# Kernel tuning notes

Hardware: AMD Instinct MI355X
Metric: run time of the kernel (lower is better)

## Reference

```python
import jax, jax.numpy as jnp
import numpy as np

N_NODES = 100000
N_EDGES = 600000
DIM = 128
NUM_CLASSES = 10
NUM_GRAPHS = 512
NUM_LAYERS = 4
BN_EPS = 1e-5


def _bn(h, g, b):
    # BatchNorm1d, training-mode statistics (biased variance), affine
    m = h.mean(axis=0)
    v = jnp.var(h, axis=0)
    return (h - m) * jax.lax.rsqrt(v + BN_EPS) * g + b


def setup_inputs() -> dict:
    key = jax.random.key(0)
    ks = jax.random.split(key, 8)
    s_in = 1.0 / np.sqrt(DIM)
    x = jax.random.normal(ks[0], (N_NODES, DIM), dtype=jnp.float32)
    edge_index = jax.random.randint(ks[1], (2, N_EDGES), 0, N_NODES, dtype=jnp.int32)
    batch = jnp.sort(jax.random.randint(ks[2], (N_NODES,), 0, NUM_GRAPHS, dtype=jnp.int32))
    return {
        "x": x,
        "edge_index": edge_index,
        "batch": batch,
        "mlp_w1": jax.random.normal(ks[3], (NUM_LAYERS, DIM, DIM), dtype=jnp.float32) * s_in,
        "mlp_b1": jnp.zeros((NUM_LAYERS, DIM), dtype=jnp.float32),
        "mlp_bn_g": jnp.ones((NUM_LAYERS, DIM), dtype=jnp.float32),
        "mlp_bn_b": jnp.zeros((NUM_LAYERS, DIM), dtype=jnp.float32),
        "mlp_w2": jax.random.normal(ks[4], (NUM_LAYERS, DIM, DIM), dtype=jnp.float32) * s_in,
        "mlp_b2": jnp.zeros((NUM_LAYERS, DIM), dtype=jnp.float32),
        "bn_g": jnp.ones((NUM_LAYERS, DIM), dtype=jnp.float32),
        "bn_b": jnp.zeros((NUM_LAYERS, DIM), dtype=jnp.float32),
        "fc_w": jax.random.normal(ks[5], (NUM_LAYERS + 1, DIM, NUM_CLASSES), dtype=jnp.float32) * s_in,
        "fc_b": jnp.zeros((NUM_LAYERS + 1, NUM_CLASSES), dtype=jnp.float32),
    }


def reference(x, edge_index, batch, mlp_w1, mlp_b1, mlp_bn_g, mlp_bn_b,
              mlp_w2, mlp_b2, bn_g, bn_b, fc_w, fc_b):
    src, dst = edge_index[0], edge_index[1]
    outs = [x]
    h = x
    for i in range(NUM_LAYERS):
        # GINConv: (1+eps)*x + sum_{j in N(i)} x_j  with eps=0 (default)
        agg = jax.ops.segment_sum(h[src], dst, num_segments=N_NODES)
        z = h + agg
        # nn.Sequential(Linear, BatchNorm1d, ReLU, Linear)
        z = jax.nn.relu(_bn(z @ mlp_w1[i] + mlp_b1[i], mlp_bn_g[i], mlp_bn_b[i]))
        z = z @ mlp_w2[i] + mlp_b2[i]
        # outer BN + ReLU
        h = jax.nn.relu(_bn(z, bn_g[i], bn_b[i]))
        outs.append(h)
    out = None
    for i, o in enumerate(outs):
        pooled = jax.ops.segment_sum(o, batch, num_segments=NUM_GRAPHS)
        y = pooled @ fc_w[i] + fc_b[i]  # dropout is identity in eval mode
        out = y if out is None else out + y
    return jax.nn.log_softmax(out, axis=-1)
```

## Files before the change

kernel.cpp:

```cpp
#include <hip/hip_runtime.h>

#define NN 100000
#define NE 600000
#define DD 128
#define NG 512
#define NC 10
#define NL 4

typedef __attribute__((ext_vector_type(8))) short short8;
typedef __attribute__((ext_vector_type(4))) float f32x4;
typedef __attribute__((ext_vector_type(4))) unsigned int u32x4;

__device__ __forceinline__ float b2f(unsigned int u) { return __uint_as_float(u << 16); }
__device__ __forceinline__ unsigned int f2b(float f) {
    unsigned int u = __float_as_uint(f);
    return (u + 0x7fffu + ((u >> 16) & 1u)) >> 16;
}
__device__ __forceinline__ void unpack8(uint4 v, float* f) {
    f[0] = b2f(v.x & 0xffffu); f[1] = b2f(v.x >> 16);
    f[2] = b2f(v.y & 0xffffu); f[3] = b2f(v.y >> 16);
    f[4] = b2f(v.z & 0xffffu); f[5] = b2f(v.z >> 16);
    f[6] = b2f(v.w & 0xffffu); f[7] = b2f(v.w >> 16);
}
__device__ __forceinline__ uint4 pack8(const float* f) {
    uint4 v;
    v.x = f2b(f[0]) | (f2b(f[1]) << 16);
    v.y = f2b(f[2]) | (f2b(f[3]) << 16);
    v.z = f2b(f[4]) | (f2b(f[5]) << 16);
    v.w = f2b(f[6]) | (f2b(f[7]) << 16);
    return v;
}
__device__ __forceinline__ void nt_store16(uint4 v, ushort* p) {
    u32x4 w = {v.x, v.y, v.z, v.w};
    __builtin_nontemporal_store(w, (u32x4*)p);
}

__device__ __forceinline__ void gload_lds16(const void* g, void* l) {
    __builtin_amdgcn_global_load_lds((__attribute__((address_space(1))) void*)g,
                                     (__attribute__((address_space(3))) void*)l, 16, 0, 0);
}

__device__ __forceinline__ void build_bnp(const float* __restrict__ st, const float* __restrict__ gma,
                                          const float* __restrict__ bta, float (*bnp)[DD], int t) {
    if (t < DD) {
        float s = 0.f, q = 0.f;
        #pragma unroll
        for (int r = 0; r < 8; ++r) { s += st[r * DD + t]; q += st[8 * DD + r * DD + t]; }
        const float invn = 1.0f / NN;
        float m = s * invn;
        float var = q * invn - m * m;
        float sc = gma[t] * rsqrtf(var + 1e-5f);
        bnp[0][t] = sc;
        bnp[1][t] = bta[t] - m * sc;
    }
}

__global__ __launch_bounds__(256) void k_init(const float* __restrict__ x, ushort* __restrict__ h,
                                              float* __restrict__ pz, int nz, int* __restrict__ deg,
                                              const float* __restrict__ w1, const float* __restrict__ w2,
                                              ushort* __restrict__ wp) {
    const int T = gridDim.x * 256;
    const int tid = blockIdx.x * 256 + threadIdx.x;
    for (int i = tid; i < NN * DD / 8; i += T) {
        float4 a = ((const float4*)x)[2 * i], b = ((const float4*)x)[2 * i + 1];
        float f[8] = {a.x, a.y, a.z, a.w, b.x, b.y, b.z, b.w};
        ((uint4*)h)[i] = pack8(f);
    }
    for (int i = tid; i < nz; i += T) pz[i] = 0.f;
    for (int i = tid; i < NN; i += T) deg[i] = 0;
    for (int id = tid; id < 16384; id += T) {
        int v = id & 63;
        int kc = (id >> 6) & 3;
        int ct = (id >> 8) & 7;
        int m = id >> 11;
        const float* W = (m < 4) ? (w1 + (size_t)m * DD * DD) : (w2 + (size_t)(m - 4) * DD * DD);
        int c = ct * 16 + (v & 15);
        int kbase = kc * 32 + ((v >> 4) << 3);
        ushort* dst = wp + ((size_t)id << 3);
        #pragma unroll
        for (int j = 0; j < 8; ++j) dst[j] = (ushort)f2b(W[(size_t)(kbase + j) * DD + c]);
    }
}


__global__ __launch_bounds__(256) void k_hist(const int* __restrict__ dst, int* __restrict__ deg) {
    int e = blockIdx.x * 256 + threadIdx.x;
    if (e < NE) atomicAdd(&deg[dst[e]], 1);
}
__global__ __launch_bounds__(256) void k_partial(const int* __restrict__ deg, int* __restrict__ part) {
    __shared__ int s[256];
    int t = threadIdx.x;
    int i = blockIdx.x * 256 + t;
    s[t] = (i < NN) ? deg[i] : 0;
    __syncthreads();
    #pragma unroll
    for (int off = 128; off >= 1; off >>= 1) {
        if (t < off) s[t] += s[t + off];
        __syncthreads();
    }
    if (t == 0) part[blockIdx.x] = s[0];
}
__global__ __launch_bounds__(512) void k_scanpart(int* __restrict__ part, int nb) {
    __shared__ int s[512];
    int t = threadIdx.x;
    int v = (t < nb) ? part[t] : 0;
    s[t] = v;
    __syncthreads();
    #pragma unroll
    for (int off = 1; off < 512; off <<= 1) {
        int add = (t >= off) ? s[t - off] : 0;
        __syncthreads();
        s[t] += add;
        __syncthreads();
    }
    if (t < nb) part[t] = s[t] - v;
}
__global__ __launch_bounds__(256) void k_exscan(const int* __restrict__ deg, const int* __restrict__ part,
                                                int* __restrict__ rowofs, int* __restrict__ cursor) {
    __shared__ int s[256];
    int b = blockIdx.x, t = threadIdx.x;
    int i = b * 256 + t;
    int v = (i < NN) ? deg[i] : 0;
    s[t] = v;
    __syncthreads();
    #pragma unroll
    for (int off = 1; off < 256; off <<= 1) {
        int add = (t >= off) ? s[t - off] : 0;
        __syncthreads();
        s[t] += add;
        __syncthreads();
    }
    if (i < NN) {
        int r = part[b] + s[t] - v;
        rowofs[i] = r;
        cursor[i] = r;
    }
    if (i == NN - 1) rowofs[NN] = part[b] + s[t];
}
__global__ __launch_bounds__(256) void k_fill(const int* __restrict__ src, const int* __restrict__ dst,
                                              int* __restrict__ cursor, int* __restrict__ csr) {
    int e = blockIdx.x * 256 + threadIdx.x;
    if (e >= NE) return;
    int d = dst[e];
    int pos = atomicAdd(&cursor[d], 1);
    csr[pos] = src[e];
}

template<bool BN>
__global__ __launch_bounds__(256) void k_gather(const int* __restrict__ rowofs, const int* __restrict__ csr,
                                                const int* __restrict__ batch,
                                                const ushort* __restrict__ h, ushort* __restrict__ z,
                                                const float* __restrict__ st, const float* __restrict__ gma,
                                                const float* __restrict__ bta,
                                                float* __restrict__ poolslot) {
    __shared__ float bnp[2][DD];
    __shared__ float sfl[16][DD];
    __shared__ int gids[16];
    int t = threadIdx.x;
    if (BN) build_bnp(st, gma, bta, bnp, t);
    int rs = t >> 4;
    int n = blockIdx.x * 16 + rs;
    int cl = t & 15;
    int cb = cl * 8;
    if (cl == 0) gids[rs] = batch[n];
    uint4 v = ((const uint4*)h)[(size_t)n * 16 + cl];
    if (BN) __syncthreads();
    float sc[8], sh[8];
    if (BN) {
        #pragma unroll
        for (int j = 0; j < 8; ++j) { sc[j] = bnp[0][cb + j]; sh[j] = bnp[1][cb + j]; }
    }
    float acc[8], f[8];
    unpack8(v, f);
    #pragma unroll
    for (int j = 0; j < 8; ++j)
        acc[j] = BN ? fmaxf(fmaf(f[j], sc[j], sh[j]), 0.f) : f[j];
    #pragma unroll
    for (int j = 0; j < 8; j += 4)
        *(float4*)(&sfl[rs][cb + j]) = make_float4(acc[j], acc[j + 1], acc[j + 2], acc[j + 3]);
    __syncthreads();
    if (t < DD) {
        float run = sfl[0][t];
        int gprev = gids[0];
        #pragma unroll
        for (int s = 1; s < 16; ++s) {
            int gg = gids[s];
            float vv = sfl[s][t];
            if (gg != gprev) {
                atomicAdd(poolslot + (size_t)gprev * DD + t, run);
                run = 0.f;
                gprev = gg;
            }
            run += vv;
        }
        atomicAdd(poolslot + (size_t)gprev * DD + t, run);
    }
    int e = rowofs[n], end = rowofs[n + 1];
    int i0 = 0, i1 = 0, i2 = 0, i3 = 0;
    if (e + 3 < end) { i0 = csr[e]; i1 = csr[e + 1]; i2 = csr[e + 2]; i3 = csr[e + 3]; }
    while (e + 3 < end) {
        uint4 v0 = ((const uint4*)h)[(size_t)i0 * 16 + cl];
        uint4 v1 = ((const uint4*)h)[(size_t)i1 * 16 + cl];
        uint4 v2 = ((const uint4*)h)[(size_t)i2 * 16 + cl];
        uint4 v3 = ((const uint4*)h)[(size_t)i3 * 16 + cl];
        int en = e + 4;
        if (en + 3 < end) {
            i0 = csr[en]; i1 = csr[en + 1]; i2 = csr[en + 2]; i3 = csr[en + 3];
        }
        float f0[8], f1[8], f2[8], f3[8];
        unpack8(v0, f0); unpack8(v1, f1); unpack8(v2, f2); unpack8(v3, f3);
        #pragma unroll
        for (int j = 0; j < 8; ++j) {
            float a0 = BN ? fmaxf(fmaf(f0[j], sc[j], sh[j]), 0.f) : f0[j];
            float a1 = BN ? fmaxf(fmaf(f1[j], sc[j], sh[j]), 0.f) : f1[j];
            float a2 = BN ? fmaxf(fmaf(f2[j], sc[j], sh[j]), 0.f) : f2[j];
            float a3 = BN ? fmaxf(fmaf(f3[j], sc[j], sh[j]), 0.f) : f3[j];
            acc[j] += (a0 + a1) + (a2 + a3);
        }
        e = en;
    }
    for (; e < end; ++e) {
        uint4 v0 = ((const uint4*)h)[(size_t)csr[e] * 16 + cl];
        float f0[8];
        unpack8(v0, f0);
        #pragma unroll
        for (int j = 0; j < 8; ++j)
            acc[j] += BN ? fmaxf(fmaf(f0[j], sc[j], sh[j]), 0.f) : f0[j];
    }
    nt_store16(pack8(acc), z + ((size_t)n * 16 + cl) * 8);
}

template<bool TRANS>
__global__ __launch_bounds__(256, 4) void k_mm(const ushort* __restrict__ in, const ushort* __restrict__ wp,
                                               const float* __restrict__ bias,
                                               const float* __restrict__ stin, const float* __restrict__ gma,
                                               const float* __restrict__ bta,
                                               ushort* __restrict__ outp, float* __restrict__ stout) {
    __shared__ __align__(16) char lds[16384];
    __shared__ float bnp[2][DD];
    const int t = threadIdx.x;
    const int lane = t & 63;
    const int wid = t >> 6;
    const int wr = wid >> 1, wc = wid & 1;
    const int rb = blockIdx.x * 64;
    const int rep = blockIdx.x & 7;

    if (TRANS) {
        build_bnp(stin, gma, bta, bnp, t);
        __syncthreads();
    }
    if (!TRANS && rb + 64 <= NN) {
        #pragma unroll
        for (int i = 0; i < 4; ++i) {
            int p = i * 256 + t;
            int row = p >> 4;
            int oc = (p & 15) ^ (row & 7);
            gload_lds16((const uint4*)in + (size_t)(rb + row) * 16 + oc, lds + p * 16);
        }
    } else {
        float scv[8], shv[8];
        if (TRANS) {
            int cb = (t & 15) * 8;
            #pragma unroll
            for (int j = 0; j < 8; ++j) { scv[j] = bnp[0][cb + j]; shv[j] = bnp[1][cb + j]; }
        }
        #pragma unroll
        for (int i = 0; i < 4; ++i) {
            int c = i * 256 + t;
            int row = c >> 4;
            int g = rb + row;
            uint4 v = make_uint4(0, 0, 0, 0);
            if (g < NN) {
                v = *((const uint4*)in + (size_t)g * 16 + (c & 15));
                if (TRANS) {
                    float f[8];
                    unpack8(v, f);
                    #pragma unroll
                    for (int j = 0; j < 8; ++j) f[j] = fmaxf(fmaf(f[j], scv[j], shv[j]), 0.f);
                    v = pack8(f);
                }
            }
            *(uint4*)(lds + ((c * 16) ^ ((row & 7) << 4))) = v;
        }
    }
    __syncthreads();

    f32x4 acc[2][4];
    #pragma unroll
    for (int rt = 0; rt < 2; ++rt)
        #pragma unroll
        for (int ct = 0; ct < 4; ++ct) acc[rt][ct] = (f32x4){0.f, 0.f, 0.f, 0.f};

    #pragma unroll
    for (int kc = 0; kc < 4; ++kc) {
        short8 wf[4];
        #pragma unroll
        for (int ct = 0; ct < 4; ++ct)
            wf[ct] = *(const short8*)(wp + (size_t)((((wc * 4 + ct) * 4 + kc) * 64 + lane) << 3));
        #pragma unroll
        for (int rt = 0; rt < 2; ++rt) {
            int row = wr * 32 + rt * 16 + (lane & 15);
            int off = (row * 256 + ((kc * 32 + ((lane >> 4) << 3)) << 1)) ^ ((row & 7) << 4);
            short8 zf = *(const short8*)(lds + off);
            #pragma unroll
            for (int ct = 0; ct < 4; ++ct)
                acc[rt][ct] = __builtin_amdgcn_mfma_f32_16x16x32_bf16(wf[ct], zf, acc[rt][ct], 0, 0, 0);
        }
    }
    __syncthreads();

    const int zr = lane & 15, cq = lane >> 4;
    #pragma unroll
    for (int rt = 0; rt < 2; ++rt) {
        int row = wr * 32 + rt * 16 + zr;
        #pragma unroll
        for (int ct = 0; ct < 4; ++ct) {
            int c0 = wc * 64 + ct * 16 + cq * 4;
            float4 bi = *(const float4*)(bias + c0);
            f32x4 a = acc[rt][ct];
            uint2 pk;
            pk.x = f2b(a[0] + bi.x) | (f2b(a[1] + bi.y) << 16);
            pk.y = f2b(a[2] + bi.z) | (f2b(a[3] + bi.w) << 16);
            *(uint2*)(lds + ((row * 256 + c0 * 2) ^ ((row & 7) << 4))) = pk;
        }
    }
    __syncthreads();

    float s8[8], q8[8];
    #pragma unroll
    for (int j = 0; j < 8; ++j) { s8[j] = 0.f; q8[j] = 0.f; }
    #pragma unroll
    for (int i = 0; i < 4; ++i) {
        int c = i * 256 + t;
        int row = c >> 4;
        int g = rb + row;
        if (g < NN) {
            uint4 v = *(const uint4*)(lds + ((c * 16) ^ ((row & 7) << 4)));
            ((uint4*)outp)[(size_t)g * 16 + (c & 15)] = v;
            float f[8];
            unpack8(v, f);
            #pragma unroll
            for (int j = 0; j < 8; ++j) { s8[j] += f[j]; q8[j] += f[j] * f[j]; }
        }
    }
    #pragma unroll
    for (int j = 0; j < 8; ++j) {
        s8[j] += __shfl_xor(s8[j], 16); s8[j] += __shfl_xor(s8[j], 32);
        q8[j] += __shfl_xor(q8[j], 16); q8[j] += __shfl_xor(q8[j], 32);
    }
    __syncthreads();
    float* rs2 = (float*)lds;
    if (lane < 16) {
        #pragma unroll
        for (int j = 0; j < 8; j += 4) {
            *(float4*)(rs2 + wid * DD + lane * 8 + j) = make_float4(s8[j], s8[j+1], s8[j+2], s8[j+3]);
            *(float4*)(rs2 + 4 * DD + wid * DD + lane * 8 + j) = make_float4(q8[j], q8[j+1], q8[j+2], q8[j+3]);
        }
    }
    __syncthreads();
    if (t < DD) {
        float s = rs2[t] + rs2[DD + t] + rs2[2 * DD + t] + rs2[3 * DD + t];
        float q = rs2[4 * DD + t] + rs2[5 * DD + t] + rs2[6 * DD + t] + rs2[7 * DD + t];
        atomicAdd(stout + rep * DD + t, s);
        atomicAdd(stout + 8 * DD + rep * DD + t, q);
    }
}

__device__ __forceinline__ int lowerb(const int* __restrict__ a, int n, int key) {
    int lo = 0, hi = n;
    while (lo < hi) {
        int mid = (lo + hi) >> 1;
        if (a[mid] < key) lo = mid + 1; else hi = mid;
    }
    return lo;
}

__global__ __launch_bounds__(256) void k_poolread(const int* __restrict__ batch, const ushort* __restrict__ h,
                                                  const float* __restrict__ pooled,
                                                  const float* __restrict__ st, const float* __restrict__ gma,
                                                  const float* __restrict__ bta,
                                                  const float* __restrict__ fcw, const float* __restrict__ fcb,
                                                  float* __restrict__ out) {
    __shared__ float bnp[2][DD];
    __shared__ float red[16 * DD];
    __shared__ float ps[2][NC];
    int t = threadIdx.x;
    build_bnp(st, gma, bta, bnp, t);
    __syncthreads();
    int g = blockIdx.x;
    int cl = t & 15;
    int rs = t >> 4;
    int cb = cl * 8;
    float sc[8], sh[8];
    #pragma unroll
    for (int j = 0; j < 8; ++j) { sc[j] = bnp[0][cb + j]; sh[j] = bnp[1][cb + j]; }
    int start = lowerb(batch, NN, g);
    int end = lowerb(batch, NN, g + 1);
    float acc[8];
    #pragma unroll
    for (int j = 0; j < 8; ++j) acc[j] = 0.f;
    for (int n = start + rs; n < end; n += 16) {
        uint4 v = ((const uint4*)h)[(size_t)n * 16 + cl];
        float f[8];
        unpack8(v, f);
        #pragma unroll
        for (int j = 0; j < 8; ++j)
            acc[j] += fmaxf(fmaf(f[j], sc[j], sh[j]), 0.f);
    }
    #pragma unroll
    for (int j = 0; j < 8; j += 4)
        *(float4*)(red + rs * DD + cb + j) = make_float4(acc[j], acc[j + 1], acc[j + 2], acc[j + 3]);
    __syncthreads();
    #pragma unroll
    for (int off = 8; off >= 1; off >>= 1) {
        if (rs < off) {
            #pragma unroll
            for (int j = 0; j < 8; j += 4) {
                float4 a = *(float4*)(red + rs * DD + cb + j);
                float4 b = *(float4*)(red + (rs + off) * DD + cb + j);
                a.x += b.x; a.y += b.y; a.z += b.z; a.w += b.w;
                *(float4*)(red + rs * DD + cb + j) = a;
            }
        }
        __syncthreads();
    }
    if (t < DD) {
        int d = t;
        float part[NC];
        #pragma unroll
        for (int c = 0; c < NC; ++c) part[c] = 0.f;
        #pragma unroll
        for (int i = 0; i < NL; ++i) {
            float v = pooled[((size_t)i * NG + g) * DD + d];
            const float* wr = fcw + ((size_t)i * DD + d) * NC;
            #pragma unroll
            for (int c = 0; c < NC; ++c) part[c] = fmaf(v, wr[c], part[c]);
        }
        {
            float v = red[d];
            const float* wr = fcw + ((size_t)NL * DD + d) * NC;
            #pragma unroll
            for (int c = 0; c < NC; ++c) part[c] = fmaf(v, wr[c], part[c]);
        }
        #pragma unroll
        for (int off = 32; off >= 1; off >>= 1) {
            #pragma unroll
            for (int c = 0; c < NC; ++c) part[c] += __shfl_down(part[c], off);
        }
        if ((t & 63) == 0) {
            #pragma unroll
            for (int c = 0; c < NC; ++c) ps[t >> 6][c] = part[c];
        }
    }
    __syncthreads();
    if (t == 0) {
        float y[NC];
        #pragma unroll
        for (int c = 0; c < NC; ++c) {
            float bs = 0.f;
            for (int i = 0; i < NL + 1; ++i) bs += fcb[i * NC + c];
            y[c] = ps[0][c] + ps[1][c] + bs;
        }
        float m = y[0];
        #pragma unroll
        for (int c = 1; c < NC; ++c) m = fmaxf(m, y[c]);
        float sum = 0.f;
        #pragma unroll
        for (int c = 0; c < NC; ++c) sum += expf(y[c] - m);
        float ls = logf(sum);
        #pragma unroll
        for (int c = 0; c < NC; ++c) out[(size_t)g * NC + c] = y[c] - m - ls;
    }
}


extern "C" void kernel_launch(void* const* d_in, const int* in_sizes, int n_in,
                              void* d_out, int out_size, void* d_ws, size_t ws_size,
                              hipStream_t stream) {
    const float* x   = (const float*)d_in[0];
    const int*   ei  = (const int*)d_in[1];
    const int*   bat = (const int*)d_in[2];
    const float* w1  = (const float*)d_in[3];
    const float* b1  = (const float*)d_in[4];
    const float* mbg = (const float*)d_in[5];
    const float* mbb = (const float*)d_in[6];
    const float* w2  = (const float*)d_in[7];
    const float* b2  = (const float*)d_in[8];
    const float* bng = (const float*)d_in[9];
    const float* bnb = (const float*)d_in[10];
    const float* fcw = (const float*)d_in[11];
    const float* fcb = (const float*)d_in[12];
    float* out = (float*)d_out;

    ushort* H  = (ushort*)d_ws;
    ushort* Z  = H + (size_t)NN * DD;
    ushort* Y1 = Z + (size_t)NN * DD;
    ushort* WP = Y1 + (size_t)NN * DD;
    float* pooled = (float*)(WP + 8 * 16384);
    float* stats  = pooled + (size_t)NL * NG * DD;
    int* deg    = (int*)(stats + 8 * 16 * DD);
    int* rowofs = deg + NN;
    int* part   = rowofs + NN + 1;
    int* cursor = part + 512;
    int* csr    = cursor + NN;

    const int* src = ei;
    const int* dst = ei + NE;
    const int nbN = (NN + 255) / 256;
    const int nbE = (NE + 255) / 256;
    const int nzero = NL * NG * DD + 8 * 16 * DD;

    hipLaunchKernelGGL(k_init, dim3(NN * DD / 8 / 256 + 1), dim3(256), 0, stream,
                       x, H, pooled, nzero, deg, w1, w2, WP);
    hipLaunchKernelGGL(k_hist, dim3(nbE), dim3(256), 0, stream, dst, deg);
    hipLaunchKernelGGL(k_partial, dim3(nbN), dim3(256), 0, stream, deg, part);
    hipLaunchKernelGGL(k_scanpart, dim3(1), dim3(512), 0, stream, part, nbN);
    hipLaunchKernelGGL(k_exscan, dim3(nbN), dim3(256), 0, stream, deg, part, rowofs, cursor);
    hipLaunchKernelGGL(k_fill, dim3(nbE), dim3(256), 0, stream, src, dst, cursor, csr);

    const int gmm = (NN + 63) / 64;
    const int ggt = NN / 16;
    const int SLOT = 16 * DD;
    for (int i = 0; i < NL; ++i) {
        float* st_mlp = stats + (size_t)(2 * i + 0) * SLOT;
        float* st_out = stats + (size_t)(2 * i + 1) * SLOT;
        const float* st_prev = stats + (size_t)(2 * i - 1) * SLOT;
        float* poolslot = pooled + (size_t)i * NG * DD;
        if (i == 0) {
            hipLaunchKernelGGL((k_gather<false>), dim3(ggt), dim3(256), 0, stream, rowofs, csr, bat, H, Z,
                               (const float*)nullptr, (const float*)nullptr, (const float*)nullptr, poolslot);
        } else {
            hipLaunchKernelGGL((k_gather<true>), dim3(ggt), dim3(256), 0, stream, rowofs, csr, bat, H, Z,
                               st_prev, bng + (size_t)(i - 1) * DD, bnb + (size_t)(i - 1) * DD, poolslot);
        }
        hipLaunchKernelGGL((k_mm<false>), dim3(gmm), dim3(256), 0, stream,
                           Z, WP + (size_t)i * 16384, b1 + (size_t)i * DD,
                           (const float*)nullptr, (const float*)nullptr, (const float*)nullptr,
                           Y1, st_mlp);
        hipLaunchKernelGGL((k_mm<true>), dim3(gmm), dim3(256), 0, stream,
                           Y1, WP + (size_t)(4 + i) * 16384, b2 + (size_t)i * DD,
                           st_mlp, mbg + (size_t)i * DD, mbb + (size_t)i * DD,
                           H, st_out);
    }
    hipLaunchKernelGGL(k_poolread, dim3(NG), dim3(256), 0, stream, bat, H, pooled,
                       stats + (size_t)7 * SLOT, bng + (size_t)3 * DD, bnb + (size_t)3 * DD,
                       fcw, fcb, out);
}
```

Baseline: 369.3 us.

## Fuse both MLP matmuls into one cooperative kernel with grid-wide BN sync

Each of the two per-layer MLP matmuls becomes one cooperative kernel. A block computes the first linear layer for 128 rows and keeps the bf16 result in LDS. A grid sync then waits for the global BatchNorm statistics, and the block applies BN plus ReLU in LDS before the second matmul. This removes the global write and re-read of the intermediate activation and one launch per layer. In exchange it needs every block resident at once, pays for a grid-wide barrier, and falls back to the two-kernel path if the cooperative launch fails.

```diff
diff --git a/kernel.cpp b/kernel.cpp
--- a/kernel.cpp
+++ b/kernel.cpp
@@ -1,4 +1,5 @@
 #include <hip/hip_runtime.h>
+#include <hip/hip_cooperative_groups.h>
 
 #define NN 100000
 #define NE 600000
@@ -6,6 +7,8 @@
 #define NG 512
 #define NC 10
 #define NL 4
+
+namespace cg = cooperative_groups;
 
 typedef __attribute__((ext_vector_type(8))) short short8;
 typedef __attribute__((ext_vector_type(4))) float f32x4;
@@ -230,6 +233,233 @@
     nt_store16(pack8(acc), z + ((size_t)n * 16 + cl) * 8);
 }
 
+__global__ __launch_bounds__(256, 4) void k_mmfused(
+        const ushort* __restrict__ zin, const ushort* __restrict__ wp1, const ushort* __restrict__ wp2,
+        const float* __restrict__ b1v, const float* __restrict__ b2v,
+        float* __restrict__ stmid, const float* __restrict__ gma, const float* __restrict__ bta,
+        ushort* __restrict__ hout, float* __restrict__ stout) {
+    __shared__ __align__(16) char lds[32768];
+    __shared__ float bnp[2][DD];
+    __shared__ float red8[8 * DD];
+    const int t = threadIdx.x;
+    const int lane = t & 63;
+    const int wid = t >> 6;
+    const int wr = wid >> 1, wc = wid & 1;
+    const int rb0 = blockIdx.x * 128;
+    const int rep = blockIdx.x & 7;
+
+    float s8[8], q8[8];
+    #pragma unroll
+    for (int j = 0; j < 8; ++j) { s8[j] = 0.f; q8[j] = 0.f; }
+
+    #pragma unroll
+    for (int s = 0; s < 2; ++s) {
+        const int rb = rb0 + s * 64;
+        char* slot = lds + s * 16384;
+        if (rb + 64 <= NN) {
+            #pragma unroll
+            for (int i = 0; i < 4; ++i) {
+                int p = i * 256 + t;
+                int row = p >> 4;
+                int oc = (p & 15) ^ (row & 7);
+                gload_lds16((const uint4*)zin + (size_t)(rb + row) * 16 + oc, slot + p * 16);
+            }
+        } else {
+            #pragma unroll
+            for (int i = 0; i < 4; ++i) {
+                int c = i * 256 + t;
+                int row = c >> 4;
+                int g = rb + row;
+                uint4 v = make_uint4(0, 0, 0, 0);
+                if (g < NN) v = *((const uint4*)zin + (size_t)g * 16 + (c & 15));
+                *(uint4*)(slot + ((c * 16) ^ ((row & 7) << 4))) = v;
+            }
+        }
+        __syncthreads();
+
+        f32x4 acc[2][4];
+        #pragma unroll
+        for (int rt = 0; rt < 2; ++rt)
+            #pragma unroll
+            for (int ct = 0; ct < 4; ++ct) acc[rt][ct] = (f32x4){0.f, 0.f, 0.f, 0.f};
+        #pragma unroll
+        for (int kc = 0; kc < 4; ++kc) {
+            short8 wf[4];
+            #pragma unroll
+            for (int ct = 0; ct < 4; ++ct)
+                wf[ct] = *(const short8*)(wp1 + (size_t)((((wc * 4 + ct) * 4 + kc) * 64 + lane) << 3));
+            #pragma unroll
+            for (int rt = 0; rt < 2; ++rt) {
+                int row = wr * 32 + rt * 16 + (lane & 15);
+                int off = (row * 256 + ((kc * 32 + ((lane >> 4) << 3)) << 1)) ^ ((row & 7) << 4);
+                short8 zf = *(const short8*)(slot + off);
+                #pragma unroll
+                for (int ct = 0; ct < 4; ++ct)
+                    acc[rt][ct] = __builtin_amdgcn_mfma_f32_16x16x32_bf16(wf[ct], zf, acc[rt][ct], 0, 0, 0);
+            }
+        }
+        __syncthreads();
+        const int zr = lane & 15, cq = lane >> 4;
+        #pragma unroll
+        for (int rt = 0; rt < 2; ++rt) {
+            int row = wr * 32 + rt * 16 + zr;
+            #pragma unroll
+            for (int ct = 0; ct < 4; ++ct) {
+                int c0 = wc * 64 + ct * 16 + cq * 4;
+                float4 bi = *(const float4*)(b1v + c0);
+                f32x4 a = acc[rt][ct];
+                uint2 pk;
+                pk.x = f2b(a[0] + bi.x) | (f2b(a[1] + bi.y) << 16);
+                pk.y = f2b(a[2] + bi.z) | (f2b(a[3] + bi.w) << 16);
+                *(uint2*)(slot + ((row * 256 + c0 * 2) ^ ((row & 7) << 4))) = pk;
+            }
+        }
+        __syncthreads();
+        #pragma unroll
+        for (int i = 0; i < 4; ++i) {
+            int c = i * 256 + t;
+            int row = c >> 4;
+            int g = rb + row;
+            if (g < NN) {
+                uint4 v = *(const uint4*)(slot + ((c * 16) ^ ((row & 7) << 4)));
+                float f[8];
+                unpack8(v, f);
+                #pragma unroll
+                for (int j = 0; j < 8; ++j) { s8[j] += f[j]; q8[j] += f[j] * f[j]; }
+            }
+        }
+    }
+    #pragma unroll
+    for (int j = 0; j < 8; ++j) {
+        s8[j] += __shfl_xor(s8[j], 16); s8[j] += __shfl_xor(s8[j], 32);
+        q8[j] += __shfl_xor(q8[j], 16); q8[j] += __shfl_xor(q8[j], 32);
+    }
+    if (lane < 16) {
+        #pragma unroll
+        for (int j = 0; j < 8; j += 4) {
+            *(float4*)(red8 + wid * DD + lane * 8 + j) = make_float4(s8[j], s8[j+1], s8[j+2], s8[j+3]);
+            *(float4*)(red8 + 4 * DD + wid * DD + lane * 8 + j) = make_float4(q8[j], q8[j+1], q8[j+2], q8[j+3]);
+        }
+    }
+    __syncthreads();
+    if (t < DD) {
+        float s = red8[t] + red8[DD + t] + red8[2 * DD + t] + red8[3 * DD + t];
+        float q = red8[4 * DD + t] + red8[5 * DD + t] + red8[6 * DD + t] + red8[7 * DD + t];
+        atomicAdd(stmid + rep * DD + t, s);
+        atomicAdd(stmid + 8 * DD + rep * DD + t, q);
+    }
+    __threadfence();
+    cg::this_grid().sync();
+
+    if (t < DD) {
+        float s = 0.f, q = 0.f;
+        #pragma unroll
+        for (int r = 0; r < 8; ++r) {
+            s += __hip_atomic_load(stmid + r * DD + t, __ATOMIC_RELAXED, __HIP_MEMORY_SCOPE_AGENT);
+            q += __hip_atomic_load(stmid + 8 * DD + r * DD + t, __ATOMIC_RELAXED, __HIP_MEMORY_SCOPE_AGENT);
+        }
+        const float invn = 1.0f / NN;
+        float m = s * invn;
+        float var = q * invn - m * m;
+        float sc = gma[t] * rsqrtf(var + 1e-5f);
+        bnp[0][t] = sc;
+        bnp[1][t] = bta[t] - m * sc;
+    }
+    __syncthreads();
+    #pragma unroll
+    for (int i = 0; i < 8; ++i) {
+        int p = i * 256 + t;
+        int cb = ((p ^ ((p >> 4) & 7)) & 15) * 8;
+        uint4 v = *(const uint4*)(lds + p * 16);
+        float f[8];
+        unpack8(v, f);
+        #pragma unroll
+        for (int j = 0; j < 8; ++j) f[j] = fmaxf(fmaf(f[j], bnp[0][cb + j], bnp[1][cb + j]), 0.f);
+        *(uint4*)(lds + p * 16) = pack8(f);
+    }
+    __syncthreads();
+
+    #pragma unroll
+    for (int j = 0; j < 8; ++j) { s8[j] = 0.f; q8[j] = 0.f; }
+    #pragma unroll
+    for (int s = 0; s < 2; ++s) {
+        const int rb = rb0 + s * 64;
+        char* slot = lds + s * 16384;
+        f32x4 acc[2][4];
+        #pragma unroll
+        for (int rt = 0; rt < 2; ++rt)
+            #pragma unroll
+            for (int ct = 0; ct < 4; ++ct) acc[rt][ct] = (f32x4){0.f, 0.f, 0.f, 0.f};
+        #pragma unroll
+        for (int kc = 0; kc < 4; ++kc) {
+            short8 wf[4];
+            #pragma unroll
+            for (int ct = 0; ct < 4; ++ct)
+                wf[ct] = *(const short8*)(wp2 + (size_t)((((wc * 4 + ct) * 4 + kc) * 64 + lane) << 3));
+            #pragma unroll
+            for (int rt = 0; rt < 2; ++rt) {
+                int row = wr * 32 + rt * 16 + (lane & 15);
+                int off = (row * 256 + ((kc * 32 + ((lane >> 4) << 3)) << 1)) ^ ((row & 7) << 4);
+                short8 zf = *(const short8*)(slot + off);
+                #pragma unroll
+                for (int ct = 0; ct < 4; ++ct)
+                    acc[rt][ct] = __builtin_amdgcn_mfma_f32_16x16x32_bf16(wf[ct], zf, acc[rt][ct], 0, 0, 0);
+            }
+        }
+        __syncthreads();
+        const int zr = lane & 15, cq = lane >> 4;
+        #pragma unroll
+        for (int rt = 0; rt < 2; ++rt) {
+            int row = wr * 32 + rt * 16 + zr;
+            #pragma unroll
+            for (int ct = 0; ct < 4; ++ct) {
+                int c0 = wc * 64 + ct * 16 + cq * 4;
+                float4 bi = *(const float4*)(b2v + c0);
+                f32x4 a = acc[rt][ct];
+                uint2 pk;
+                pk.x = f2b(a[0] + bi.x) | (f2b(a[1] + bi.y) << 16);
+                pk.y = f2b(a[2] + bi.z) | (f2b(a[3] + bi.w) << 16);
+                *(uint2*)(slot + ((row * 256 + c0 * 2) ^ ((row & 7) << 4))) = pk;
+            }
+        }
+        __syncthreads();
+        #pragma unroll
+        for (int i = 0; i < 4; ++i) {
+            int c = i * 256 + t;
+            int row = c >> 4;
+            int g = rb + row;
+            if (g < NN) {
+                uint4 v = *(const uint4*)(slot + ((c * 16) ^ ((row & 7) << 4)));
+                ((uint4*)hout)[(size_t)g * 16 + (c & 15)] = v;
+                float f[8];
+                unpack8(v, f);
+                #pragma unroll
+                for (int j = 0; j < 8; ++j) { s8[j] += f[j]; q8[j] += f[j] * f[j]; }
+            }
+        }
+        __syncthreads();
+    }
+    #pragma unroll
+    for (int j = 0; j < 8; ++j) {
+        s8[j] += __shfl_xor(s8[j], 16); s8[j] += __shfl_xor(s8[j], 32);
+        q8[j] += __shfl_xor(q8[j], 16); q8[j] += __shfl_xor(q8[j], 32);
+    }
+    if (lane < 16) {
+        #pragma unroll
+        for (int j = 0; j < 8; j += 4) {
+            *(float4*)(red8 + wid * DD + lane * 8 + j) = make_float4(s8[j], s8[j+1], s8[j+2], s8[j+3]);
+            *(float4*)(red8 + 4 * DD + wid * DD + lane * 8 + j) = make_float4(q8[j], q8[j+1], q8[j+2], q8[j+3]);
+        }
+    }
+    __syncthreads();
+    if (t < DD) {
+        float s = red8[t] + red8[DD + t] + red8[2 * DD + t] + red8[3 * DD + t];
+        float q = red8[4 * DD + t] + red8[5 * DD + t] + red8[6 * DD + t] + red8[7 * DD + t];
+        atomicAdd(stout + rep * DD + t, s);
+        atomicAdd(stout + 8 * DD + rep * DD + t, q);
+    }
+}
+
 template<bool TRANS>
 __global__ __launch_bounds__(256, 4) void k_mm(const ushort* __restrict__ in, const ushort* __restrict__ wp,
                                                const float* __restrict__ bias,
@@ -519,6 +749,7 @@
     hipLaunchKernelGGL(k_fill, dim3(nbE), dim3(256), 0, stream, src, dst, cursor, csr);
 
     const int gmm = (NN + 63) / 64;
+    const int gfu = (NN + 127) / 128;
     const int ggt = NN / 16;
     const int SLOT = 16 * DD;
     for (int i = 0; i < NL; ++i) {
@@ -533,14 +764,29 @@
             hipLaunchKernelGGL((k_gather<true>), dim3(ggt), dim3(256), 0, stream, rowofs, csr, bat, H, Z,
                                st_prev, bng + (size_t)(i - 1) * DD, bnb + (size_t)(i - 1) * DD, poolslot);
         }
-        hipLaunchKernelGGL((k_mm<false>), dim3(gmm), dim3(256), 0, stream,
-                           Z, WP + (size_t)i * 16384, b1 + (size_t)i * DD,
-                           (const float*)nullptr, (const float*)nullptr, (const float*)nullptr,
-                           Y1, st_mlp);
-        hipLaunchKernelGGL((k_mm<true>), dim3(gmm), dim3(256), 0, stream,
-                           Y1, WP + (size_t)(4 + i) * 16384, b2 + (size_t)i * DD,
-                           st_mlp, mbg + (size_t)i * DD, mbb + (size_t)i * DD,
-                           H, st_out);
+        {
+            const ushort* zf = Z;
+            const ushort* wp1 = WP + (size_t)i * 16384;
+            const ushort* wp2 = WP + (size_t)(4 + i) * 16384;
+            const float* b1p = b1 + (size_t)i * DD;
+            const float* b2p = b2 + (size_t)i * DD;
+            float* stmid = st_mlp;
+            const float* gmap = mbg + (size_t)i * DD;
+            const float* btap = mbb + (size_t)i * DD;
+            ushort* hp = H;
+            float* stoutp = st_out;
+            void* args[] = {&zf, &wp1, &wp2, &b1p, &b2p, &stmid, &gmap, &btap, &hp, &stoutp};
+            hipError_t rc = hipLaunchCooperativeKernel((const void*)k_mmfused, dim3(gfu), dim3(256),
+                                                       args, 0, stream);
+            if (rc != hipSuccess) {
+                hipLaunchKernelGGL((k_mm<false>), dim3(gmm), dim3(256), 0, stream,
+                                   Z, wp1, b1p,
+                                   (const float*)nullptr, (const float*)nullptr, (const float*)nullptr,
+                                   Y1, st_mlp);
+                hipLaunchKernelGGL((k_mm<true>), dim3(gmm), dim3(256), 0, stream,
+                                   Y1, wp2, b2p, st_mlp, gmap, btap, H, st_out);
+            }
+        }
     }
     hipLaunchKernelGGL(k_poolread, dim3(NG), dim3(256), 0, stream, bat, H, pooled,
                        stats + (size_t)7 * SLOT, bng + (size_t)3 * DD, bnb + (size_t)3 * DD,
```

After: 1.023 ms. 2.77x slower.
